# Kernel tuning notes

Hardware: AMD Instinct MI355X
Metric: run time of the kernel (lower is better)

Reference implementation:

```python
import jax, jax.numpy as jnp
import numpy as np

B, T, S, H, N = 4, 1024, 1024, 1024, 16
D = H // N
EPS = 1e-12
MASK_FILL = -1e6


def setup_inputs() -> dict:
    key = jax.random.key(0)
    ks = jax.random.split(key, 20)
    w = lambda i: jax.random.normal(ks[i], (H, H), jnp.float32) * 0.02
    zb = jnp.zeros((H,), jnp.float32)
    tgt_mask = jnp.tile(jnp.tril(jnp.ones((T, T), jnp.int32))[None], (B, 1, 1))
    return {
        "encoder_states": jax.random.normal(ks[0], (B, S, H), jnp.float32),
        "decoder_inputs": jax.random.normal(ks[1], (B, T, H), jnp.float32),
        "src_attn_mask": jnp.ones((B, S), jnp.int32),
        "tgt_attn_mask": tgt_mask,
        "q_w": w(2), "q_b": zb,
        "k_w": w(3), "k_b": zb,
        "v_w": w(4), "v_b": zb,
        "sq_w": w(5), "sq_b": zb,
        "sk_w": w(6), "sk_b": zb,
        "sv_w": w(7), "sv_b": zb,
        "dense_w": w(8), "dense_b": zb,
        "ln_g": jnp.ones((H,), jnp.float32),
        "ln_b": zb,
    }


def _layernorm(x, g, b):
    mu = jnp.mean(x, -1, keepdims=True)
    var = jnp.mean(jnp.square(x - mu), -1, keepdims=True)
    return (x - mu) * jax.lax.rsqrt(var + EPS) * g + b


def _attention(q, k, v, mask, dense_w, dense_b, ln_g, ln_b):
    # q:[B,Q,H] k,v:[B,K,H]; NOTE: original applies NO 1/sqrt(d) scaling.
    b, qlen, _ = q.shape
    klen = k.shape[1]
    qh = q.reshape(b, qlen, N, D).transpose(0, 2, 1, 3)  # [B,N,Q,D]
    kh = k.reshape(b, klen, N, D).transpose(0, 2, 1, 3)
    vh = v.reshape(b, klen, N, D).transpose(0, 2, 1, 3)
    scores = jnp.einsum('bnqd,bnkd->bnqk', qh, kh)
    m = mask.reshape(b, 1, qlen, klen) if mask.ndim == 3 else mask.reshape(b, 1, 1, klen)
    scores = jnp.where(m == 0, jnp.asarray(MASK_FILL, scores.dtype), scores)
    probs = jax.nn.softmax(scores, axis=-1)  # dropout = identity at eval
    ctx = jnp.einsum('bnqk,bnkd->bqnd', probs, vh)  # [B,Q,N,D]
    w = dense_w.T.reshape(N, D, H)
    proj = jnp.einsum('bqnd,ndh->bqh', ctx, w) + dense_b
    # Residual is q (the query projection), faithful to the original code.
    return _layernorm(q + proj, ln_g, ln_b)


def reference(encoder_states, decoder_inputs, src_attn_mask, tgt_attn_mask,
              q_w, q_b, k_w, k_b, v_w, v_b,
              sq_w, sq_b, sk_w, sk_b, sv_w, sv_b,
              dense_w, dense_b, ln_g, ln_b):
    lin = lambda x, w, b: x @ w.T + b
    # self-attention over decoder inputs
    q = lin(decoder_inputs, q_w, q_b)
    k = lin(decoder_inputs, k_w, k_b)
    v = lin(decoder_inputs, v_w, v_b)
    self_out = _attention(q, k, v, tgt_attn_mask, dense_w, dense_b, ln_g, ln_b)
    # cross-attention into encoder states (same dense/LayerNorm modules)
    q2 = lin(self_out, sq_w, sq_b)
    k2 = lin(encoder_states, sk_w, sk_b)
    v2 = lin(encoder_states, sv_w, sv_b)
    return _attention(q2, k2, v2, src_attn_mask, dense_w, dense_b, ln_g, ln_b)
```

## Files before the change

### kernel.cpp

```cpp
#include <hip/hip_runtime.h>

typedef __attribute__((ext_vector_type(4))) float f32x4;
typedef __attribute__((ext_vector_type(8))) short bf16x8;

#define GVOID const __attribute__((address_space(1))) void
#define LVOID __attribute__((address_space(3))) void

#define LOG2E 1.44269504f
#define LN2   0.69314718f

__device__ __forceinline__ float bf2f(ushort u){
  union { float f; unsigned int i; } c; c.i = ((unsigned int)u) << 16; return c.f;
}
__device__ __forceinline__ ushort f2bf(float f){
  union { float f; unsigned int i; } c; c.f = f;
  unsigned int r = (c.i + 0x7FFFu + ((c.i >> 16) & 1u)) >> 16;
  return (ushort)r;
}

struct CvtArgs {
  const float* s[9];
  ushort*      d[9];
  int          blks[9];
};
__global__ __launch_bounds__(256) void cvtk_multi(CvtArgs ca){
  int bid = blockIdx.x;
  int seg = 0, base = 0;
  while (bid - base >= ca.blks[seg]){ base += ca.blks[seg]; ++seg; }
  int i = ((bid - base) * 256 + threadIdx.x) * 4;
  float4 v = *(const float4*)(ca.s[seg] + i);
  ushort4 o;
  o.x = f2bf(v.x); o.y = f2bf(v.y); o.z = f2bf(v.z); o.w = f2bf(v.w);
  *(ushort4*)(ca.d[seg] + i) = o;
}

struct GemmArgs {
  const ushort* A[3];
  const ushort* W[3];
  const float*  bias[3];
  const ushort* R[3];
  ushort*       C[3];
  int           mode[3];
  float         scale[3];
};

__global__ __launch_bounds__(256,2) void gemm128(GemmArgs ga, int nmat, int N, int K){
  __shared__ ushort As[128 * 64];
  __shared__ ushort Bs[128 * 64];
  const int ntn = N >> 7;
  const int per = ntn * nmat;
  const int x = blockIdx.x & 7, ii = blockIdx.x >> 3;
  const int ipx = gridDim.x >> 3;
  const int gpx = ipx / per;
  const int tm = x * gpx + ii / per;
  const int q = ii % per;
  const int g = q / ntn, tn = q % ntn;
  const ushort* __restrict__ A = ga.A[g];
  const ushort* __restrict__ W = ga.W[g];
  const float*  __restrict__ bias = ga.bias[g];
  ushort* __restrict__ C = ga.C[g];
  const int mode = ga.mode[g];
  const float scale = ga.scale[g];

  const int t = threadIdx.x, lane = t & 63, wave = t >> 6;
  const int wr = wave >> 1, wc = wave & 1;
  const int l15 = lane & 15, l4 = lane >> 4;
  const int rowBase = tm * 128, colBase = tn * 128;

  f32x4 acc[4][4] = {};
  const int NT = K >> 6;
  for (int tk = 0; tk < NT; ++tk){
    const int k0 = tk * 64;
    __syncthreads();
#pragma unroll
    for (int j = 0; j < 4; ++j){
      int cb = j * 256 + wave * 64 + lane;
      int row = cb >> 3;
      int kc = (cb & 7) ^ (row & 7);
      const ushort* srcA = A + (size_t)(rowBase + row) * K + k0 + kc * 8;
      __builtin_amdgcn_global_load_lds((GVOID*)srcA, (LVOID*)(As + (size_t)cb * 8), 16, 0, 0);
      const ushort* srcB = W + (size_t)(colBase + row) * K + k0 + kc * 8;
      __builtin_amdgcn_global_load_lds((GVOID*)srcB, (LVOID*)(Bs + (size_t)cb * 8), 16, 0, 0);
    }
    __syncthreads();
#pragma unroll
    for (int kk = 0; kk < 2; ++kk){
      bf16x8 a[4], b[4];
#pragma unroll
      for (int m = 0; m < 4; ++m){
        int row = wr * 64 + m * 16 + l15;
        int ch = row * 8 + ((kk * 4 + l4) ^ (row & 7));
        a[m] = *(const bf16x8*)(As + ch * 8);
      }
#pragma unroll
      for (int n = 0; n < 4; ++n){
        int row = wc * 64 + n * 16 + l15;
        int ch = row * 8 + ((kk * 4 + l4) ^ (row & 7));
        b[n] = *(const bf16x8*)(Bs + ch * 8);
      }
#pragma unroll
      for (int m = 0; m < 4; ++m)
#pragma unroll
      for (int n = 0; n < 4; ++n)
        acc[m][n] = __builtin_amdgcn_mfma_f32_16x16x32_bf16(a[m], b[n], acc[m][n], 0, 0, 0);
    }
  }
#pragma unroll
  for (int m = 0; m < 4; ++m)
#pragma unroll
  for (int n = 0; n < 4; ++n)
#pragma unroll
  for (int r = 0; r < 4; ++r){
    int row = rowBase + wr * 64 + m * 16 + l4 * 4 + r;
    int col = colBase + wc * 64 + n * 16 + l15;
    float v = (acc[m][n][r] + bias[col]) * scale;
    if (mode == 2){
      int bb = row >> 10, tt = row & 1023, nh = col >> 6, d = col & 63;
      C[((size_t)((bb * 16 + nh) * 64 + d)) * 1024 + tt] = f2bf(v);
    } else {
      C[(size_t)row * N + col] = f2bf(v);
    }
  }
}

__global__ __launch_bounds__(256,2) void gemm_bt(GemmArgs ga, int nmat, int M, int N, int K){
  __shared__ ushort As[2][128 * 64];
  __shared__ ushort Bs[2][64 * 64];
  const int nb = gridDim.x;
  const int ntn = N >> 6;
  const int tq_cnt = ntn * nmat;
  const int x = blockIdx.x & 7, ii = blockIdx.x >> 3;
  const int ipx = nb >> 3;
  const int gpx = ipx / tq_cnt;
  const int tm = x * gpx + ii / tq_cnt;
  const int tq = ii % tq_cnt;
  const int g = tq / ntn, tn = tq % ntn;
  const ushort* __restrict__ A = ga.A[g];
  const ushort* __restrict__ W = ga.W[g];
  const float*  __restrict__ bias = ga.bias[g];
  const ushort* __restrict__ R = ga.R[g];
  ushort* __restrict__ C = ga.C[g];
  const int mode = ga.mode[g];

  const int t = threadIdx.x, lane = t & 63, wave = t >> 6;
  const int wr = wave >> 1, wc = wave & 1;
  const int l15 = lane & 15, l4 = lane >> 4;
  const int rowBase = tm * 128, colBase = tn * 64;

  auto stage = [&](int buf, int k0){
#pragma unroll
    for (int j = 0; j < 4; ++j){
      int cb = j * 256 + wave * 64;
      int p = cb + lane;
      int row = p >> 3;
      int kc = (p & 7) ^ (row & 7);
      const ushort* src = A + (size_t)(rowBase + row) * K + k0 + kc * 8;
      __builtin_amdgcn_global_load_lds((GVOID*)src, (LVOID*)(&As[buf][cb * 8]), 16, 0, 0);
    }
#pragma unroll
    for (int j = 0; j < 2; ++j){
      int cb = j * 256 + wave * 64;
      int p = cb + lane;
      int row = p >> 3;
      int kc = (p & 7) ^ (row & 7);
      const ushort* src = W + (size_t)(colBase + row) * K + k0 + kc * 8;
      __builtin_amdgcn_global_load_lds((GVOID*)src, (LVOID*)(&Bs[buf][cb * 8]), 16, 0, 0);
    }
  };

  f32x4 acc[4][2] = {};
  const int NT = K >> 6;
  stage(0, 0);
  __syncthreads();
  for (int tk = 0; tk < NT; ++tk){
    const int cur = tk & 1;
    if (tk + 1 < NT) stage(cur ^ 1, (tk + 1) * 64);
#pragma unroll
    for (int kk = 0; kk < 2; ++kk){
      bf16x8 a[4], b[2];
#pragma unroll
      for (int m = 0; m < 4; ++m){
        int row = wr * 64 + m * 16 + l15;
        int ch = row * 8 + kk * 4 + l4;
        ch ^= (row & 7);
        a[m] = *(const bf16x8*)(&As[cur][ch * 8]);
      }
#pragma unroll
      for (int n = 0; n < 2; ++n){
        int row = wc * 32 + n * 16 + l15;
        int ch = row * 8 + kk * 4 + l4;
        ch ^= (row & 7);
        b[n] = *(const bf16x8*)(&Bs[cur][ch * 8]);
      }
#pragma unroll
      for (int m = 0; m < 4; ++m)
#pragma unroll
      for (int n = 0; n < 2; ++n)
        acc[m][n] = __builtin_amdgcn_mfma_f32_16x16x32_bf16(a[m], b[n], acc[m][n], 0, 0, 0);
    }
    __syncthreads();
  }
#pragma unroll
  for (int m = 0; m < 4; ++m)
#pragma unroll
  for (int n = 0; n < 2; ++n)
#pragma unroll
  for (int r = 0; r < 4; ++r){
    int row = rowBase + wr * 64 + m * 16 + l4 * 4 + r;
    int col = colBase + wc * 32 + n * 16 + l15;
    float v = acc[m][n][r] + bias[col];
    if (mode == 1) v += bf2f(R[(size_t)row * N + col]) * LN2;
    C[(size_t)row * N + col] = f2bf(v);
  }
}

__global__ __launch_bounds__(256,4) void attn_kernel(const ushort* __restrict__ Q, const ushort* __restrict__ Kv,
    const ushort* __restrict__ Vt, ushort* __restrict__ O, const int* __restrict__ smask, int causal){
  __shared__ ushort Ks[2][64 * 64];
  __shared__ ushort Vs[2][64 * 64];
  __shared__ __align__(16) char Ps[4][2048];
  const int p = blockIdx.x;
  const int x = p & 7, j = p >> 3;
  const int gg = x * 8 + (j & 7);
  const int b = gg >> 4, head = gg & 15;
  const int rr = j >> 3;
  int qt;
  if (causal){
    int lo = rr & 3, hi = rr >> 2;
    qt = (hi == 0) ? lo * 2 : (hi == 1) ? lo * 2 + 1 : (hi == 2) ? 15 - lo * 2 : 14 - lo * 2;
  } else qt = rr;
  const int t = threadIdx.x, lane = t & 63, wave = t >> 6;
  const int l15 = lane & 15, l4 = lane >> 4;
  const int qr0 = qt * 64 + wave * 16;
  const int sw = (l15 & 7) << 3;

  bf16x8 aq[2];
#pragma unroll
  for (int kk = 0; kk < 2; ++kk)
    aq[kk] = *(const bf16x8*)(Q + (size_t)(b * 1024 + qr0 + l15) * 1024 + head * 64 + kk * 32 + l4 * 8);

  f32x4 cacc[4] = {};
  float mrow = -1e30f, lrow = 0.f;

  auto stage = [&](int buf, int k0){
#pragma unroll
    for (int jj = 0; jj < 2; ++jj){
      int cb = jj * 256 + wave * 64;
      int pp = cb + lane;
      int row = pp >> 3;
      int kc = (pp & 7) ^ (row & 7);
      const ushort* src = Kv + (size_t)(b * 1024 + k0 + row) * 1024 + head * 64 + kc * 8;
      __builtin_amdgcn_global_load_lds((GVOID*)src, (LVOID*)(&Ks[buf][cb * 8]), 16, 0, 0);
    }
#pragma unroll
    for (int jj = 0; jj < 2; ++jj){
      int cb = jj * 256 + wave * 64;
      int pp = cb + lane;
      int row = pp >> 3;
      int kc = (pp & 7) ^ (row & 7);
      const ushort* src = Vt + (size_t)((b * 16 + head) * 64 + row) * 1024 + k0 + kc * 8;
      __builtin_amdgcn_global_load_lds((GVOID*)src, (LVOID*)(&Vs[buf][cb * 8]), 16, 0, 0);
    }
  };

  const int nkt = causal ? (qt + 1) : 16;
  stage(0, 0);
  __syncthreads();
  char* Pb = &Ps[wave][0];
  for (int kt = 0; kt < nkt; ++kt){
    const int cur = kt & 1;
    const int k0 = kt * 64;
    if (kt + 1 < nkt) stage(cur ^ 1, (kt + 1) * 64);
    const ushort* Kb_ = &Ks[cur][0];
    const ushort* Vb_ = &Vs[cur][0];
    f32x4 st[4] = {};
#pragma unroll
    for (int kk = 0; kk < 2; ++kk){
      bf16x8 ak[4];
#pragma unroll
      for (int n = 0; n < 4; ++n){
        int row = n * 16 + l15;
        int ch = row * 8 + ((kk * 4 + l4) ^ (row & 7));
        ak[n] = *(const bf16x8*)(Kb_ + ch * 8);
      }
#pragma unroll
      for (int n = 0; n < 4; ++n)
        st[n] = __builtin_amdgcn_mfma_f32_16x16x32_bf16(ak[n], aq[kk], st[n], 0, 0, 0);
    }
    if (causal && k0 + 63 > qr0){
#pragma unroll
      for (int n = 0; n < 4; ++n)
#pragma unroll
      for (int r = 0; r < 4; ++r)
        if (k0 + n * 16 + l4 * 4 + r > qr0 + l15) st[n][r] = -1.5e6f;
    }
    if (smask){
#pragma unroll
      for (int n = 0; n < 4; ++n)
#pragma unroll
      for (int r = 0; r < 4; ++r){
        int mv = smask[b * 1024 + k0 + n * 16 + l4 * 4 + r];
        if (mv == 0) st[n][r] = -1.5e6f;
      }
    }
    float mx = st[0][0];
#pragma unroll
    for (int n = 0; n < 4; ++n)
#pragma unroll
    for (int r = 0; r < 4; ++r) mx = fmaxf(mx, st[n][r]);
    mx = fmaxf(mx, __shfl_xor(mx, 16));
    mx = fmaxf(mx, __shfl_xor(mx, 32));
    float mn = fmaxf(mrow, mx);
    float scal = __builtin_amdgcn_exp2f(mrow - mn);
    mrow = mn;
    float ps = 0.f;
#pragma unroll
    for (int n = 0; n < 4; ++n)
#pragma unroll
    for (int r = 0; r < 4; ++r){
      float pv = __builtin_amdgcn_exp2f(st[n][r] - mn);
      st[n][r] = pv;
      ps += pv;
    }
    ps += __shfl_xor(ps, 16);
    ps += __shfl_xor(ps, 32);
    lrow = lrow * scal + ps;
#pragma unroll
    for (int r = 0; r < 4; ++r){
      float sb = __shfl(scal, l4 * 4 + r);
#pragma unroll
      for (int nd = 0; nd < 4; ++nd) cacc[nd][r] *= sb;
    }
#pragma unroll
    for (int n = 0; n < 4; ++n){
      unsigned lo_, hi_;
      asm("v_cvt_pk_bf16_f32 %0, %1, %2" : "=v"(lo_) : "v"(st[n][0]), "v"(st[n][1]));
      asm("v_cvt_pk_bf16_f32 %0, %1, %2" : "=v"(hi_) : "v"(st[n][2]), "v"(st[n][3]));
      unsigned long long pk = (unsigned long long)lo_ | ((unsigned long long)hi_ << 32);
      *(unsigned long long*)(Pb + l15 * 128 + ((n * 32 + l4 * 8) ^ sw)) = pk;
    }
#pragma unroll
    for (int ks = 0; ks < 2; ++ks){
      bf16x8 bv[4];
#pragma unroll
      for (int nd = 0; nd < 4; ++nd){
        int row = nd * 16 + l15;
        int ch = row * 8 + ((ks * 4 + l4) ^ (row & 7));
        bv[nd] = *(const bf16x8*)(Vb_ + ch * 8);
      }
      int base = l15 * 128;
      int o = ks * 64 + l4 * 16;
      union { bf16x8 v; unsigned long long u[2]; } pa;
      pa.u[0] = *(const unsigned long long*)(Pb + base + ((o    ) ^ sw));
      pa.u[1] = *(const unsigned long long*)(Pb + base + ((o + 8) ^ sw));
#pragma unroll
      for (int nd = 0; nd < 4; ++nd)
        cacc[nd] = __builtin_amdgcn_mfma_f32_16x16x32_bf16(pa.v, bv[nd], cacc[nd], 0, 0, 0);
    }
    __syncthreads();
  }
#pragma unroll
  for (int r = 0; r < 4; ++r){
    float lb = __shfl(lrow, l4 * 4 + r);
    float inv = 1.f / lb;
    int row = qr0 + l4 * 4 + r;
#pragma unroll
    for (int nd = 0; nd < 4; ++nd){
      int col = head * 64 + nd * 16 + l15;
      O[(size_t)(b * 1024 + row) * 1024 + col] = f2bf(cacc[nd][r] * inv);
    }
  }
}

__global__ __launch_bounds__(256) void ln_kernel(const ushort* __restrict__ X, const float* __restrict__ g,
    const float* __restrict__ bta, ushort* __restrict__ outb, float* __restrict__ outf){
  const int row = blockIdx.x, t = threadIdx.x;
  const ushort* xr = X + (size_t)row * 1024;
  ushort4 u = *(const ushort4*)(xr + t * 4);
  float x0 = bf2f(u.x), x1 = bf2f(u.y), x2 = bf2f(u.z), x3 = bf2f(u.w);
  float s = x0 + x1 + x2 + x3;
  float s2 = x0 * x0 + x1 * x1 + x2 * x2 + x3 * x3;
#pragma unroll
  for (int d = 1; d < 64; d <<= 1){ s += __shfl_xor(s, d); s2 += __shfl_xor(s2, d); }
  __shared__ float red[8];
  const int lane = t & 63, wave = t >> 6;
  if (lane == 0){ red[wave] = s; red[4 + wave] = s2; }
  __syncthreads();
  s = red[0] + red[1] + red[2] + red[3];
  s2 = red[4] + red[5] + red[6] + red[7];
  float mu = s * (1.f / 1024.f);
  float var = fmaxf(s2 * (1.f / 1024.f) - mu * mu, 0.f);
  float rstd = rsqrtf(var + 1e-12f);
  int col = t * 4;
  float y0 = (x0 - mu) * rstd * g[col + 0] + bta[col + 0];
  float y1 = (x1 - mu) * rstd * g[col + 1] + bta[col + 1];
  float y2 = (x2 - mu) * rstd * g[col + 2] + bta[col + 2];
  float y3 = (x3 - mu) * rstd * g[col + 3] + bta[col + 3];
  if (outb){
    ushort4 o; o.x = f2bf(y0); o.y = f2bf(y1); o.z = f2bf(y2); o.w = f2bf(y3);
    *(ushort4*)(outb + (size_t)row * 1024 + col) = o;
  } else {
    float4 o; o.x = y0; o.y = y1; o.z = y2; o.w = y3;
    *(float4*)(outf + (size_t)row * 1024 + col) = o;
  }
}

extern "C" void kernel_launch(void* const* d_in, const int* in_sizes, int n_in,
                              void* d_out, int out_size, void* d_ws, size_t ws_size,
                              hipStream_t stream){
  const float* enc = (const float*)d_in[0];
  const float* dec = (const float*)d_in[1];
  const int* smask = (const int*)d_in[2];
  const float* q_w  = (const float*)d_in[4];  const float* q_b  = (const float*)d_in[5];
  const float* k_w  = (const float*)d_in[6];  const float* k_b  = (const float*)d_in[7];
  const float* v_w  = (const float*)d_in[8];  const float* v_b  = (const float*)d_in[9];
  const float* sq_w = (const float*)d_in[10]; const float* sq_b = (const float*)d_in[11];
  const float* sk_w = (const float*)d_in[12]; const float* sk_b = (const float*)d_in[13];
  const float* sv_w = (const float*)d_in[14]; const float* sv_b = (const float*)d_in[15];
  const float* dw   = (const float*)d_in[16]; const float* db   = (const float*)d_in[17];
  const float* lng  = (const float*)d_in[18]; const float* lnb  = (const float*)d_in[19];
  ushort* ws = (ushort*)d_ws;
  const size_t MEG = 1024u * 1024u;
  ushort* decb = ws + 0 * MEG;
  ushort* encb = ws + 4 * MEG;
  ushort* Qb   = ws + 8 * MEG;
  ushort* Kb   = ws + 12 * MEG;
  ushort* Vtb  = ws + 20 * MEG;
  ushort* ctx  = ws + 24 * MEG;
  ushort* S1   = ws + 28 * MEG;
  ushort* Wq  = ws + 32 * MEG; ushort* Wk  = ws + 33 * MEG; ushort* Wv  = ws + 34 * MEG;
  ushort* Wsq = ws + 35 * MEG; ushort* Wsk = ws + 36 * MEG; ushort* Wsv = ws + 37 * MEG;
  ushort* Wd  = ws + 38 * MEG;
  const int M = 4096, N = 1024, Kd = 1024;
  {
    CvtArgs ca;
    ca.s[0] = dec;  ca.d[0] = decb; ca.blks[0] = 4096;
    ca.s[1] = enc;  ca.d[1] = encb; ca.blks[1] = 4096;
    ca.s[2] = q_w;  ca.d[2] = Wq;   ca.blks[2] = 1024;
    ca.s[3] = k_w;  ca.d[3] = Wk;   ca.blks[3] = 1024;
    ca.s[4] = v_w;  ca.d[4] = Wv;   ca.blks[4] = 1024;
    ca.s[5] = sq_w; ca.d[5] = Wsq;  ca.blks[5] = 1024;
    ca.s[6] = sk_w; ca.d[6] = Wsk;  ca.blks[6] = 1024;
    ca.s[7] = sv_w; ca.d[7] = Wsv;  ca.blks[7] = 1024;
    ca.s[8] = dw;   ca.d[8] = Wd;   ca.blks[8] = 1024;
    cvtk_multi<<<15360, 256, 0, stream>>>(ca);
  }
  {
    GemmArgs ga;
    ga.A[0] = decb; ga.A[1] = decb; ga.A[2] = decb;
    ga.W[0] = Wq;   ga.W[1] = Wk;   ga.W[2] = Wv;
    ga.bias[0] = q_b; ga.bias[1] = k_b; ga.bias[2] = v_b;
    ga.R[0] = nullptr; ga.R[1] = nullptr; ga.R[2] = nullptr;
    ga.C[0] = Qb;   ga.C[1] = Kb;   ga.C[2] = Vtb;
    ga.mode[0] = 0; ga.mode[1] = 0; ga.mode[2] = 2;
    ga.scale[0] = LOG2E; ga.scale[1] = 1.f; ga.scale[2] = 1.f;
    gemm128<<<768, 256, 0, stream>>>(ga, 3, N, Kd);
  }
  attn_kernel<<<1024, 256, 0, stream>>>(Qb, Kb, Vtb, ctx, nullptr, 1);
  {
    GemmArgs ga = {};
    ga.A[0] = ctx; ga.W[0] = Wd; ga.bias[0] = db; ga.R[0] = Qb; ga.C[0] = S1; ga.mode[0] = 1;
    ga.scale[0] = 1.f;
    gemm_bt<<<512, 256, 0, stream>>>(ga, 1, M, N, Kd);
  }
  ln_kernel<<<4096, 256, 0, stream>>>(S1, lng, lnb, decb, nullptr);
  {
    GemmArgs ga;
    ga.A[0] = decb; ga.A[1] = encb; ga.A[2] = encb;
    ga.W[0] = Wsq;  ga.W[1] = Wsk;  ga.W[2] = Wsv;
    ga.bias[0] = sq_b; ga.bias[1] = sk_b; ga.bias[2] = sv_b;
    ga.R[0] = nullptr; ga.R[1] = nullptr; ga.R[2] = nullptr;
    ga.C[0] = Qb;   ga.C[1] = Kb;   ga.C[2] = Vtb;
    ga.mode[0] = 0; ga.mode[1] = 0; ga.mode[2] = 2;
    ga.scale[0] = LOG2E; ga.scale[1] = 1.f; ga.scale[2] = 1.f;
    gemm128<<<768, 256, 0, stream>>>(ga, 3, N, Kd);
  }
  attn_kernel<<<1024, 256, 0, stream>>>(Qb, Kb, Vtb, ctx, smask, 0);
  {
    GemmArgs ga = {};
    ga.A[0] = ctx; ga.W[0] = Wd; ga.bias[0] = db; ga.R[0] = Qb; ga.C[0] = S1; ga.mode[0] = 1;
    ga.scale[0] = 1.f;
    gemm_bt<<<512, 256, 0, stream>>>(ga, 1, M, N, Kd);
  }
  ln_kernel<<<4096, 256, 0, stream>>>(S1, lng, lnb, nullptr, (float*)d_out);
}
```

Baseline: 213.0 us.

## Batch cross-attention K/V projections into first GEMM using pipelined 256-tile kernel

Replaces the 128x128 QKV GEMM with a 256x256-tile, 512-thread kernel that keeps a 4-deep LDS ring of global-to-LDS loads and waits on explicit vmcnt counts. The encoder K/V projections do not depend on the self-attention output, so they move into this first launch as five matrices in one grid, writing to new workspace buffers. The later cross-attention Q projection now runs alone through gemm_bt, which gains a scale parameter. The goal is to cut launch count, raise data reuse per tile and overlap loads with MFMA work. In exchange, 320 large blocks using 128 KB of LDS each fit one per CU and leave an uneven tail wave, and the workspace grows.

```diff
diff --git a/kernel.cpp b/kernel.cpp
--- a/kernel.cpp
+++ b/kernel.cpp
@@ -34,6 +34,105 @@
   *(ushort4*)(ca.d[seg] + i) = o;
 }
 
+struct Gemm5Args {
+  const ushort* A[5];
+  const ushort* W[5];
+  const float*  bias[5];
+  ushort*       C[5];
+  int           mode[5];
+  float         scale[5];
+};
+
+__global__ __launch_bounds__(512,2) void gemm256(Gemm5Args ga, int nmat, int K){
+  __shared__ ushort AS[4][8192];
+  __shared__ ushort BS[4][8192];
+  const int per = nmat * 4;
+  const int x = blockIdx.x & 7, ii = blockIdx.x >> 3;
+  const int gpx = (gridDim.x >> 3) / per;
+  const int tm = x * gpx + ii / per;
+  const int tq = ii % per;
+  const int g = tq >> 2, tn = tq & 3;
+  const ushort* __restrict__ A = ga.A[g];
+  const ushort* __restrict__ W = ga.W[g];
+  const float*  __restrict__ bias = ga.bias[g];
+  ushort* __restrict__ C = ga.C[g];
+  const int mode = ga.mode[g];
+  const float scale = ga.scale[g];
+
+  const int t = threadIdx.x, lane = t & 63, wave = t >> 6;
+  const int wr = wave >> 2, wc = wave & 3;
+  const int l15 = lane & 15, l4 = lane >> 4;
+  const int rowBase = tm * 256, colBase = tn * 256;
+
+  auto stage = [&](int T){
+    const int slot = T & 3;
+    const int k0 = T << 5;
+#pragma unroll
+    for (int i = 0; i < 2; ++i){
+      int cb = i * 512 + t;
+      int row = cb >> 2;
+      int kc = (cb & 3) ^ ((row >> 1) & 3);
+      const ushort* srcA = A + (size_t)(rowBase + row) * K + k0 + kc * 8;
+      __builtin_amdgcn_global_load_lds((GVOID*)srcA, (LVOID*)(&AS[slot][cb * 8]), 16, 0, 0);
+      const ushort* srcB = W + (size_t)(colBase + row) * K + k0 + kc * 8;
+      __builtin_amdgcn_global_load_lds((GVOID*)srcB, (LVOID*)(&BS[slot][cb * 8]), 16, 0, 0);
+    }
+  };
+
+  f32x4 acc[8][4] = {};
+  const int NT = K >> 5;
+  stage(0); stage(1); stage(2);
+  for (int T = 0; T < NT; ++T){
+    if (T + 3 < NT) stage(T + 3);
+    const int rem = NT - 1 - T;
+    if (rem >= 3)      asm volatile("s_waitcnt vmcnt(12)" ::: "memory");
+    else if (rem == 2) asm volatile("s_waitcnt vmcnt(8)"  ::: "memory");
+    else if (rem == 1) asm volatile("s_waitcnt vmcnt(4)"  ::: "memory");
+    else               asm volatile("s_waitcnt vmcnt(0)"  ::: "memory");
+    __builtin_amdgcn_s_barrier();
+    const ushort* As_ = &AS[T & 3][0];
+    const ushort* Bs_ = &BS[T & 3][0];
+    bf16x8 a[8], b[4];
+#pragma unroll
+    for (int m = 0; m < 8; ++m){
+      int row = wr * 128 + m * 16 + l15;
+      int ch = (row << 2) + (l4 ^ ((row >> 1) & 3));
+      a[m] = *(const bf16x8*)(As_ + ch * 8);
+    }
+#pragma unroll
+    for (int n = 0; n < 4; ++n){
+      int row = wc * 64 + n * 16 + l15;
+      int ch = (row << 2) + (l4 ^ ((row >> 1) & 3));
+      b[n] = *(const bf16x8*)(Bs_ + ch * 8);
+    }
+#pragma unroll
+    for (int m = 0; m < 8; ++m)
+#pragma unroll
+    for (int n = 0; n < 4; ++n)
+      acc[m][n] = __builtin_amdgcn_mfma_f32_16x16x32_bf16(a[m], b[n], acc[m][n], 0, 0, 0);
+    asm volatile("s_waitcnt lgkmcnt(0)" ::: "memory");
+    __builtin_amdgcn_s_barrier();
+  }
+#pragma unroll
+  for (int m = 0; m < 8; ++m)
+#pragma unroll
+  for (int n = 0; n < 4; ++n){
+    int colm = colBase + wc * 64 + n * 16 + l15;
+    float bi = bias[colm];
+#pragma unroll
+    for (int r = 0; r < 4; ++r){
+      int row = rowBase + wr * 128 + m * 16 + l4 * 4 + r;
+      float v = (acc[m][n][r] + bi) * scale;
+      if (mode == 2){
+        int bb = row >> 10, tt = row & 1023, nh = colm >> 6, d = colm & 63;
+        C[((size_t)((bb * 16 + nh) * 64 + d)) * 1024 + tt] = f2bf(v);
+      } else {
+        C[(size_t)row * 1024 + colm] = f2bf(v);
+      }
+    }
+  }
+}
+
 struct GemmArgs {
   const ushort* A[3];
   const ushort* W[3];
@@ -43,85 +142,6 @@
   int           mode[3];
   float         scale[3];
 };
-
-__global__ __launch_bounds__(256,2) void gemm128(GemmArgs ga, int nmat, int N, int K){
-  __shared__ ushort As[128 * 64];
-  __shared__ ushort Bs[128 * 64];
-  const int ntn = N >> 7;
-  const int per = ntn * nmat;
-  const int x = blockIdx.x & 7, ii = blockIdx.x >> 3;
-  const int ipx = gridDim.x >> 3;
-  const int gpx = ipx / per;
-  const int tm = x * gpx + ii / per;
-  const int q = ii % per;
-  const int g = q / ntn, tn = q % ntn;
-  const ushort* __restrict__ A = ga.A[g];
-  const ushort* __restrict__ W = ga.W[g];
-  const float*  __restrict__ bias = ga.bias[g];
-  ushort* __restrict__ C = ga.C[g];
-  const int mode = ga.mode[g];
-  const float scale = ga.scale[g];
-
-  const int t = threadIdx.x, lane = t & 63, wave = t >> 6;
-  const int wr = wave >> 1, wc = wave & 1;
-  const int l15 = lane & 15, l4 = lane >> 4;
-  const int rowBase = tm * 128, colBase = tn * 128;
-
-  f32x4 acc[4][4] = {};
-  const int NT = K >> 6;
-  for (int tk = 0; tk < NT; ++tk){
-    const int k0 = tk * 64;
-    __syncthreads();
-#pragma unroll
-    for (int j = 0; j < 4; ++j){
-      int cb = j * 256 + wave * 64 + lane;
-      int row = cb >> 3;
-      int kc = (cb & 7) ^ (row & 7);
-      const ushort* srcA = A + (size_t)(rowBase + row) * K + k0 + kc * 8;
-      __builtin_amdgcn_global_load_lds((GVOID*)srcA, (LVOID*)(As + (size_t)cb * 8), 16, 0, 0);
-      const ushort* srcB = W + (size_t)(colBase + row) * K + k0 + kc * 8;
-      __builtin_amdgcn_global_load_lds((GVOID*)srcB, (LVOID*)(Bs + (size_t)cb * 8), 16, 0, 0);
-    }
-    __syncthreads();
-#pragma unroll
-    for (int kk = 0; kk < 2; ++kk){
-      bf16x8 a[4], b[4];
-#pragma unroll
-      for (int m = 0; m < 4; ++m){
-        int row = wr * 64 + m * 16 + l15;
-        int ch = row * 8 + ((kk * 4 + l4) ^ (row & 7));
-        a[m] = *(const bf16x8*)(As + ch * 8);
-      }
-#pragma unroll
-      for (int n = 0; n < 4; ++n){
-        int row = wc * 64 + n * 16 + l15;
-        int ch = row * 8 + ((kk * 4 + l4) ^ (row & 7));
-        b[n] = *(const bf16x8*)(Bs + ch * 8);
-      }
-#pragma unroll
-      for (int m = 0; m < 4; ++m)
-#pragma unroll
-      for (int n = 0; n < 4; ++n)
-        acc[m][n] = __builtin_amdgcn_mfma_f32_16x16x32_bf16(a[m], b[n], acc[m][n], 0, 0, 0);
-    }
-  }
-#pragma unroll
-  for (int m = 0; m < 4; ++m)
-#pragma unroll
-  for (int n = 0; n < 4; ++n)
-#pragma unroll
-  for (int r = 0; r < 4; ++r){
-    int row = rowBase + wr * 64 + m * 16 + l4 * 4 + r;
-    int col = colBase + wc * 64 + n * 16 + l15;
-    float v = (acc[m][n][r] + bias[col]) * scale;
-    if (mode == 2){
-      int bb = row >> 10, tt = row & 1023, nh = col >> 6, d = col & 63;
-      C[((size_t)((bb * 16 + nh) * 64 + d)) * 1024 + tt] = f2bf(v);
-    } else {
-      C[(size_t)row * N + col] = f2bf(v);
-    }
-  }
-}
 
 __global__ __launch_bounds__(256,2) void gemm_bt(GemmArgs ga, int nmat, int M, int N, int K){
   __shared__ ushort As[2][128 * 64];
@@ -141,6 +161,7 @@
   const ushort* __restrict__ R = ga.R[g];
   ushort* __restrict__ C = ga.C[g];
   const int mode = ga.mode[g];
+  const float scale = ga.scale[g];
 
   const int t = threadIdx.x, lane = t & 63, wave = t >> 6;
   const int wr = wave >> 1, wc = wave & 1;
@@ -208,7 +229,7 @@
   for (int r = 0; r < 4; ++r){
     int row = rowBase + wr * 64 + m * 16 + l4 * 4 + r;
     int col = colBase + wc * 32 + n * 16 + l15;
-    float v = acc[m][n][r] + bias[col];
+    float v = (acc[m][n][r] + bias[col]) * scale;
     if (mode == 1) v += bf2f(R[(size_t)row * N + col]) * LN2;
     C[(size_t)row * N + col] = f2bf(v);
   }
@@ -425,12 +446,14 @@
   ushort* encb = ws + 4 * MEG;
   ushort* Qb   = ws + 8 * MEG;
   ushort* Kb   = ws + 12 * MEG;
+  ushort* K2b  = ws + 16 * MEG;
   ushort* Vtb  = ws + 20 * MEG;
   ushort* ctx  = ws + 24 * MEG;
   ushort* S1   = ws + 28 * MEG;
   ushort* Wq  = ws + 32 * MEG; ushort* Wk  = ws + 33 * MEG; ushort* Wv  = ws + 34 * MEG;
   ushort* Wsq = ws + 35 * MEG; ushort* Wsk = ws + 36 * MEG; ushort* Wsv = ws + 37 * MEG;
   ushort* Wd  = ws + 38 * MEG;
+  ushort* Vt2b = ws + 39 * MEG;
   const int M = 4096, N = 1024, Kd = 1024;
   {
     CvtArgs ca;
@@ -446,15 +469,14 @@
     cvtk_multi<<<15360, 256, 0, stream>>>(ca);
   }
   {
-    GemmArgs ga;
-    ga.A[0] = decb; ga.A[1] = decb; ga.A[2] = decb;
-    ga.W[0] = Wq;   ga.W[1] = Wk;   ga.W[2] = Wv;
-    ga.bias[0] = q_b; ga.bias[1] = k_b; ga.bias[2] = v_b;
-    ga.R[0] = nullptr; ga.R[1] = nullptr; ga.R[2] = nullptr;
-    ga.C[0] = Qb;   ga.C[1] = Kb;   ga.C[2] = Vtb;
-    ga.mode[0] = 0; ga.mode[1] = 0; ga.mode[2] = 2;
-    ga.scale[0] = LOG2E; ga.scale[1] = 1.f; ga.scale[2] = 1.f;
-    gemm128<<<768, 256, 0, stream>>>(ga, 3, N, Kd);
+    Gemm5Args ga;
+    ga.A[0] = decb; ga.A[1] = decb; ga.A[2] = decb; ga.A[3] = encb; ga.A[4] = encb;
+    ga.W[0] = Wq;   ga.W[1] = Wk;   ga.W[2] = Wv;   ga.W[3] = Wsk;  ga.W[4] = Wsv;
+    ga.bias[0] = q_b; ga.bias[1] = k_b; ga.bias[2] = v_b; ga.bias[3] = sk_b; ga.bias[4] = sv_b;
+    ga.C[0] = Qb;   ga.C[1] = Kb;   ga.C[2] = Vtb;  ga.C[3] = K2b;  ga.C[4] = Vt2b;
+    ga.mode[0] = 0; ga.mode[1] = 0; ga.mode[2] = 2; ga.mode[3] = 0; ga.mode[4] = 2;
+    ga.scale[0] = LOG2E; ga.scale[1] = 1.f; ga.scale[2] = 1.f; ga.scale[3] = 1.f; ga.scale[4] = 1.f;
+    gemm256<<<320, 512, 0, stream>>>(ga, 5, Kd);
   }
   attn_kernel<<<1024, 256, 0, stream>>>(Qb, Kb, Vtb, ctx, nullptr, 1);
   {
@@ -465,17 +487,12 @@
   }
   ln_kernel<<<4096, 256, 0, stream>>>(S1, lng, lnb, decb, nullptr);
   {
-    GemmArgs ga;
-    ga.A[0] = decb; ga.A[1] = encb; ga.A[2] = encb;
-    ga.W[0] = Wsq;  ga.W[1] = Wsk;  ga.W[2] = Wsv;
-    ga.bias[0] = sq_b; ga.bias[1] = sk_b; ga.bias[2] = sv_b;
-    ga.R[0] = nullptr; ga.R[1] = nullptr; ga.R[2] = nullptr;
-    ga.C[0] = Qb;   ga.C[1] = Kb;   ga.C[2] = Vtb;
-    ga.mode[0] = 0; ga.mode[1] = 0; ga.mode[2] = 2;
-    ga.scale[0] = LOG2E; ga.scale[1] = 1.f; ga.scale[2] = 1.f;
-    gemm128<<<768, 256, 0, stream>>>(ga, 3, N, Kd);
-  }
-  attn_kernel<<<1024, 256, 0, stream>>>(Qb, Kb, Vtb, ctx, smask, 0);
+    GemmArgs ga = {};
+    ga.A[0] = decb; ga.W[0] = Wsq; ga.bias[0] = sq_b; ga.C[0] = Qb; ga.mode[0] = 0;
+    ga.scale[0] = LOG2E;
+    gemm_bt<<<512, 256, 0, stream>>>(ga, 1, M, N, Kd);
+  }
+  attn_kernel<<<1024, 256, 0, stream>>>(Qb, K2b, Vt2b, ctx, smask, 0);
   {
     GemmArgs ga = {};
     ga.A[0] = ctx; ga.W[0] = Wd; ga.bias[0] = db; ga.R[0] = Qb; ga.C[0] = S1; ga.mode[0] = 1;
```

Measured after the change: 262.1 us. +23.1%, slower.

## Triple-buffer QKV projection GEMM with K=32 stages and vmcnt-based waits

Applied to the files above, without the earlier changes.

Replaces the single-buffered 128x128 QKV GEMM, which synchronised around each 64-wide K tile, with a three-slot ring of 32-wide K tiles. Tiles are prefetched two steps ahead with global_load_lds, and s_waitcnt vmcnt lets compute overlap outstanding loads. It raises the occupancy hint from 2 to 3 blocks per CU, hoists the bias load out of the row loop, and hardcodes N=1024. This trades more barriers per K and hand-counted waitcnt correctness for hiding global memory latency. gemm_bt also gains a scale multiply, which is 1 at its call sites.

```diff
diff --git a/kernel.cpp b/kernel.cpp
--- a/kernel.cpp
+++ b/kernel.cpp
@@ -44,17 +44,16 @@
   float         scale[3];
 };
 
-__global__ __launch_bounds__(256,2) void gemm128(GemmArgs ga, int nmat, int N, int K){
-  __shared__ ushort As[128 * 64];
-  __shared__ ushort Bs[128 * 64];
-  const int ntn = N >> 7;
+__global__ __launch_bounds__(256,3) void gemm128r(GemmArgs ga, int nmat, int K){
+  __shared__ ushort AS[3][128 * 32];
+  __shared__ ushort BS[3][128 * 32];
+  const int ntn = 8;
   const int per = ntn * nmat;
   const int x = blockIdx.x & 7, ii = blockIdx.x >> 3;
-  const int ipx = gridDim.x >> 3;
-  const int gpx = ipx / per;
+  const int gpx = (gridDim.x >> 3) / per;
   const int tm = x * gpx + ii / per;
-  const int q = ii % per;
-  const int g = q / ntn, tn = q % ntn;
+  const int tq = ii % per;
+  const int g = tq / ntn, tn = tq % ntn;
   const ushort* __restrict__ A = ga.A[g];
   const ushort* __restrict__ W = ga.W[g];
   const float*  __restrict__ bias = ga.bias[g];
@@ -67,58 +66,75 @@
   const int l15 = lane & 15, l4 = lane >> 4;
   const int rowBase = tm * 128, colBase = tn * 128;
 
+  auto stage = [&](int T, int slot){
+    const int k0 = T << 5;
+#pragma unroll
+    for (int i = 0; i < 2; ++i){
+      int cb = i * 256 + t;
+      int row = cb >> 2;
+      int kc = (cb & 3) ^ ((row >> 1) & 3);
+      const ushort* srcA = A + (size_t)(rowBase + row) * K + k0 + kc * 8;
+      __builtin_amdgcn_global_load_lds((GVOID*)srcA, (LVOID*)(&AS[slot][cb * 8]), 16, 0, 0);
+      const ushort* srcB = W + (size_t)(colBase + row) * K + k0 + kc * 8;
+      __builtin_amdgcn_global_load_lds((GVOID*)srcB, (LVOID*)(&BS[slot][cb * 8]), 16, 0, 0);
+    }
+  };
+
   f32x4 acc[4][4] = {};
-  const int NT = K >> 6;
-  for (int tk = 0; tk < NT; ++tk){
-    const int k0 = tk * 64;
-    __syncthreads();
-#pragma unroll
-    for (int j = 0; j < 4; ++j){
-      int cb = j * 256 + wave * 64 + lane;
-      int row = cb >> 3;
-      int kc = (cb & 7) ^ (row & 7);
-      const ushort* srcA = A + (size_t)(rowBase + row) * K + k0 + kc * 8;
-      __builtin_amdgcn_global_load_lds((GVOID*)srcA, (LVOID*)(As + (size_t)cb * 8), 16, 0, 0);
-      const ushort* srcB = W + (size_t)(colBase + row) * K + k0 + kc * 8;
-      __builtin_amdgcn_global_load_lds((GVOID*)srcB, (LVOID*)(Bs + (size_t)cb * 8), 16, 0, 0);
-    }
-    __syncthreads();
-#pragma unroll
-    for (int kk = 0; kk < 2; ++kk){
-      bf16x8 a[4], b[4];
-#pragma unroll
-      for (int m = 0; m < 4; ++m){
-        int row = wr * 64 + m * 16 + l15;
-        int ch = row * 8 + ((kk * 4 + l4) ^ (row & 7));
-        a[m] = *(const bf16x8*)(As + ch * 8);
+  const int NT = K >> 5;
+  stage(0, 0); stage(1, 1);
+  int slot = 0;
+  for (int T = 0; T < NT; ++T){
+    if (T + 2 < NT){
+      int s2 = slot + 2; if (s2 >= 3) s2 -= 3;
+      stage(T + 2, s2);
+      asm volatile("s_waitcnt vmcnt(8)" ::: "memory");
+    } else if (T + 1 < NT){
+      asm volatile("s_waitcnt vmcnt(4)" ::: "memory");
+    } else {
+      asm volatile("s_waitcnt vmcnt(0)" ::: "memory");
+    }
+    __builtin_amdgcn_s_barrier();
+    const ushort* As_ = &AS[slot][0];
+    const ushort* Bs_ = &BS[slot][0];
+    bf16x8 a[4], b[4];
+#pragma unroll
+    for (int m = 0; m < 4; ++m){
+      int row = wr * 64 + m * 16 + l15;
+      int ch = (row << 2) + (l4 ^ ((row >> 1) & 3));
+      a[m] = *(const bf16x8*)(As_ + ch * 8);
+    }
+#pragma unroll
+    for (int n = 0; n < 4; ++n){
+      int row = wc * 64 + n * 16 + l15;
+      int ch = (row << 2) + (l4 ^ ((row >> 1) & 3));
+      b[n] = *(const bf16x8*)(Bs_ + ch * 8);
+    }
+#pragma unroll
+    for (int m = 0; m < 4; ++m)
+#pragma unroll
+    for (int n = 0; n < 4; ++n)
+      acc[m][n] = __builtin_amdgcn_mfma_f32_16x16x32_bf16(a[m], b[n], acc[m][n], 0, 0, 0);
+    asm volatile("s_waitcnt lgkmcnt(0)" ::: "memory");
+    __builtin_amdgcn_s_barrier();
+    slot = slot == 2 ? 0 : slot + 1;
+  }
+#pragma unroll
+  for (int m = 0; m < 4; ++m)
+#pragma unroll
+  for (int n = 0; n < 4; ++n){
+    int colm = colBase + wc * 64 + n * 16 + l15;
+    float bi = bias[colm];
+#pragma unroll
+    for (int r = 0; r < 4; ++r){
+      int row = rowBase + wr * 64 + m * 16 + l4 * 4 + r;
+      float v = (acc[m][n][r] + bi) * scale;
+      if (mode == 2){
+        int bb = row >> 10, tt = row & 1023, nh = colm >> 6, d = colm & 63;
+        C[((size_t)((bb * 16 + nh) * 64 + d)) * 1024 + tt] = f2bf(v);
+      } else {
+        C[(size_t)row * 1024 + colm] = f2bf(v);
       }
-#pragma unroll
-      for (int n = 0; n < 4; ++n){
-        int row = wc * 64 + n * 16 + l15;
-        int ch = row * 8 + ((kk * 4 + l4) ^ (row & 7));
-        b[n] = *(const bf16x8*)(Bs + ch * 8);
-      }
-#pragma unroll
-      for (int m = 0; m < 4; ++m)
-#pragma unroll
-      for (int n = 0; n < 4; ++n)
-        acc[m][n] = __builtin_amdgcn_mfma_f32_16x16x32_bf16(a[m], b[n], acc[m][n], 0, 0, 0);
-    }
-  }
-#pragma unroll
-  for (int m = 0; m < 4; ++m)
-#pragma unroll
-  for (int n = 0; n < 4; ++n)
-#pragma unroll
-  for (int r = 0; r < 4; ++r){
-    int row = rowBase + wr * 64 + m * 16 + l4 * 4 + r;
-    int col = colBase + wc * 64 + n * 16 + l15;
-    float v = (acc[m][n][r] + bias[col]) * scale;
-    if (mode == 2){
-      int bb = row >> 10, tt = row & 1023, nh = col >> 6, d = col & 63;
-      C[((size_t)((bb * 16 + nh) * 64 + d)) * 1024 + tt] = f2bf(v);
-    } else {
-      C[(size_t)row * N + col] = f2bf(v);
     }
   }
 }
@@ -141,6 +157,7 @@
   const ushort* __restrict__ R = ga.R[g];
   ushort* __restrict__ C = ga.C[g];
   const int mode = ga.mode[g];
+  const float scale = ga.scale[g];
 
   const int t = threadIdx.x, lane = t & 63, wave = t >> 6;
   const int wr = wave >> 1, wc = wave & 1;
@@ -208,7 +225,7 @@
   for (int r = 0; r < 4; ++r){
     int row = rowBase + wr * 64 + m * 16 + l4 * 4 + r;
     int col = colBase + wc * 32 + n * 16 + l15;
-    float v = acc[m][n][r] + bias[col];
+    float v = (acc[m][n][r] + bias[col]) * scale;
     if (mode == 1) v += bf2f(R[(size_t)row * N + col]) * LN2;
     C[(size_t)row * N + col] = f2bf(v);
   }
@@ -446,15 +463,14 @@
     cvtk_multi<<<15360, 256, 0, stream>>>(ca);
   }
   {
-    GemmArgs ga;
+    GemmArgs ga = {};
     ga.A[0] = decb; ga.A[1] = decb; ga.A[2] = decb;
     ga.W[0] = Wq;   ga.W[1] = Wk;   ga.W[2] = Wv;
     ga.bias[0] = q_b; ga.bias[1] = k_b; ga.bias[2] = v_b;
-    ga.R[0] = nullptr; ga.R[1] = nullptr; ga.R[2] = nullptr;
     ga.C[0] = Qb;   ga.C[1] = Kb;   ga.C[2] = Vtb;
     ga.mode[0] = 0; ga.mode[1] = 0; ga.mode[2] = 2;
     ga.scale[0] = LOG2E; ga.scale[1] = 1.f; ga.scale[2] = 1.f;
-    gemm128<<<768, 256, 0, stream>>>(ga, 3, N, Kd);
+    gemm128r<<<768, 256, 0, stream>>>(ga, 3, Kd);
   }
   attn_kernel<<<1024, 256, 0, stream>>>(Qb, Kb, Vtb, ctx, nullptr, 1);
   {
@@ -465,15 +481,14 @@
   }
   ln_kernel<<<4096, 256, 0, stream>>>(S1, lng, lnb, decb, nullptr);
   {
-    GemmArgs ga;
+    GemmArgs ga = {};
     ga.A[0] = decb; ga.A[1] = encb; ga.A[2] = encb;
     ga.W[0] = Wsq;  ga.W[1] = Wsk;  ga.W[2] = Wsv;
     ga.bias[0] = sq_b; ga.bias[1] = sk_b; ga.bias[2] = sv_b;
-    ga.R[0] = nullptr; ga.R[1] = nullptr; ga.R[2] = nullptr;
     ga.C[0] = Qb;   ga.C[1] = Kb;   ga.C[2] = Vtb;
     ga.mode[0] = 0; ga.mode[1] = 0; ga.mode[2] = 2;
     ga.scale[0] = LOG2E; ga.scale[1] = 1.f; ga.scale[2] = 1.f;
-    gemm128<<<768, 256, 0, stream>>>(ga, 3, N, Kd);
+    gemm128r<<<768, 256, 0, stream>>>(ga, 3, Kd);
   }
   attn_kernel<<<1024, 256, 0, stream>>>(Qb, Kb, Vtb, ctx, smask, 0);
   {
```

Result: slower. 221.9 us (+4.2%).
